# Kernel tuning notes

Measured on AMD Instinct MI355X. Metric: run time of the kernel, lower is better.

The kernel has to match this reference:

```python
import jax, jax.numpy as jnp
import numpy as np

NEG_SLOPE = 0.2  # PyG GATConv default leaky_relu slope
EPS = 1e-16


def setup_inputs() -> dict:
    key = jax.random.key(0)
    ks = jax.random.split(key, 8)
    N, E, F = 50000, 1600000, 128
    L, H, C = 3, 4, 32  # layers, heads, per-head channels; H*C == F
    Dh = 32             # MLP hidden (== hidden_channels)
    x = jax.random.normal(ks[0], (N, F), jnp.float32)
    edge_index = jax.random.randint(ks[1], (2, E), 0, N, jnp.int32)
    W = jax.random.normal(ks[2], (L, F, H * C), jnp.float32) * 0.1
    att_src = jax.random.normal(ks[3], (L, H, C), jnp.float32) * 0.1
    att_dst = jax.random.normal(ks[4], (L, H, C), jnp.float32) * 0.1
    b_conv = jnp.zeros((L, H * C), jnp.float32)
    W1 = jax.random.normal(ks[5], (F + H * C, Dh), jnp.float32) * 0.1
    b1 = jnp.zeros((Dh,), jnp.float32)
    W2 = jax.random.normal(ks[6], (Dh, 1), jnp.float32) * 0.1
    b2 = jnp.zeros((1,), jnp.float32)
    return {"x": x, "edge_index": edge_index, "W": W, "att_src": att_src,
            "att_dst": att_dst, "b_conv": b_conv, "W1": W1, "b1": b1,
            "W2": W2, "b2": b2}


def _gat_layer(x, src, dst, W, a_s, a_d, b, N):
    H, C = a_s.shape
    h = (x @ W).reshape(N, H, C)                      # [N,H,C]
    alpha_s = jnp.sum(h * a_s, axis=-1)               # [N,H]
    alpha_d = jnp.sum(h * a_d, axis=-1)               # [N,H]
    e = jax.nn.leaky_relu(alpha_s[src] + alpha_d[dst], NEG_SLOPE)  # [E,H]
    # segment softmax over incoming edges of each dst node
    m = jax.ops.segment_max(e, dst, num_segments=N)
    ex = jnp.exp(e - m[dst])
    s = jax.ops.segment_sum(ex, dst, num_segments=N)
    a = ex / (s[dst] + EPS)                           # [E,H]
    out = jax.ops.segment_sum(h[src] * a[:, :, None], dst, num_segments=N)
    return out.reshape(N, H * C) + b


def reference(x, edge_index, W, att_src, att_dst, b_conv, W1, b1, W2, b2):
    N = x.shape[0]
    loops = jnp.arange(N, dtype=edge_index.dtype)
    src = jnp.concatenate([edge_index[0], loops])  # PyG GATConv adds self loops
    dst = jnp.concatenate([edge_index[1], loops])
    x0 = x
    for l in range(W.shape[0]):
        x = _gat_layer(x, src, dst, W[l], att_src[l], att_dst[l], b_conv[l], N)
    h = jnp.concatenate([x, x0], axis=-1)
    h = jax.nn.relu(h @ W1 + b1)
    return jax.nn.sigmoid(h @ W2 + b2)
```

## Files before the change

### kernel.cpp

```cpp
#include <hip/hip_runtime.h>

#define NEG_SLOPE 0.2f
#define EPSF 1e-16f

typedef unsigned int uint;
typedef unsigned short ushort;
typedef __attribute__((ext_vector_type(8))) short short8;
typedef __attribute__((ext_vector_type(4))) float floatx4;

static __device__ __forceinline__ ushort f2bf(float f) {
    uint u = __float_as_uint(f);
    return (ushort)((u + 0x7FFFu + ((u >> 16) & 1u)) >> 16);
}
static __device__ __forceinline__ uint pack2(float a, float b) {
    return (uint)f2bf(a) | ((uint)f2bf(b) << 16);
}
static __device__ __forceinline__ float bf_lo(uint p) { return __uint_as_float(p << 16); }
static __device__ __forceinline__ float bf_hi(uint p) { return __uint_as_float(p & 0xFFFF0000u); }
static __device__ __forceinline__ short8 u2s8(uint4 v) {
    union { uint4 u; short8 s; } c; c.u = v; return c.s;
}

__global__ __launch_bounds__(256) void prepack_w_kernel(
    const float* __restrict__ W, const float* __restrict__ W1,
    uint4* __restrict__ Wp, uint4* __restrict__ W1p, int L)
{
    int id = blockIdx.x * 256 + threadIdx.x;
    int nW = L * 2048;
    if (id < nW) {
        int l = id >> 11, s = id & 2047;
        int chunk = s >> 7, col = s & 127;
        const float* wp = W + (size_t)l * 16384 + (chunk * 8) * 128 + col;
        uint4 pk;
        pk.x = pack2(wp[0],   wp[128]);
        pk.y = pack2(wp[256], wp[384]);
        pk.z = pack2(wp[512], wp[640]);
        pk.w = pack2(wp[768], wp[896]);
        Wp[id] = pk;
    } else if (id < nW + 1024) {
        int s = id - nW;
        int chunk = s >> 5, col = s & 31;
        const float* wp = W1 + (chunk * 8) * 32 + col;
        uint4 pk;
        pk.x = pack2(wp[0],   wp[32]);
        pk.y = pack2(wp[64],  wp[96]);
        pk.z = pack2(wp[128], wp[160]);
        pk.w = pack2(wp[192], wp[224]);
        W1p[s] = pk;
    }
}

__global__ __launch_bounds__(256) void prepack_x_kernel(
    const float* __restrict__ x, uint4* __restrict__ xb, int N)
{
    int id = blockIdx.x * 256 + threadIdx.x;
    if (id >= N * 16) return;
    int row = id >> 4, c8 = id & 15;
    const float4* xp = (const float4*)(x + (size_t)row * 128 + c8 * 8);
    float4 v0 = xp[0], v1 = xp[1];
    uint4 pk;
    pk.x = pack2(v0.x, v0.y); pk.y = pack2(v0.z, v0.w);
    pk.z = pack2(v1.x, v1.y); pk.w = pack2(v1.z, v1.w);
    xb[id] = pk;
}

#define GA_LDS_BYTES ((2048 + 1040) * 16)
__global__ __launch_bounds__(256) void gemm_alpha_kernel(
    const uint4* __restrict__ xb, const uint4* __restrict__ Wp,
    const float* __restrict__ att_s, const float* __restrict__ att_d,
    uint* __restrict__ h2, float* __restrict__ alpha_s,
    float* __restrict__ alpha_d, int N)
{
    __shared__ __align__(16) char smraw[GA_LDS_BYTES];
    uint4* sW = (uint4*)smraw;
    uint4* sX = sW + 2048;
    float* sD = (float*)smraw;

    const int t = threadIdx.x;
    const int rowBase = blockIdx.x * 64;

#pragma unroll
    for (int i = 0; i < 8; ++i) {
        int slot = t + i * 256;
        sW[slot] = Wp[slot];
    }
#pragma unroll
    for (int i = 0; i < 4; ++i) {
        int f = t + i * 256;
        int row = f >> 4, c8 = f & 15;
        uint4 v = make_uint4(0u, 0u, 0u, 0u);
        if (rowBase + row < N) v = xb[(size_t)(rowBase + row) * 16 + c8];
        sX[c8 * 65 + row] = v;
    }
    __syncthreads();

    const int w = t >> 6, lane = t & 63, q = lane >> 4, l15 = lane & 15;
    short8 a[4];
#pragma unroll
    for (int s = 0; s < 4; ++s)
        a[s] = u2s8(sX[(4 * s + q) * 65 + 16 * w + l15]);

    floatx4 acc[8];
#pragma unroll
    for (int ct = 0; ct < 8; ++ct) acc[ct] = (floatx4){0.f, 0.f, 0.f, 0.f};
#pragma unroll
    for (int ct = 0; ct < 8; ++ct) {
#pragma unroll
        for (int s = 0; s < 4; ++s) {
            short8 b = u2s8(sW[(4 * s + q) * 128 + 16 * ct + l15]);
            acc[ct] = __builtin_amdgcn_mfma_f32_16x16x32_bf16(a[s], b, acc[ct], 0, 0, 0);
        }
    }
    __syncthreads();

#pragma unroll
    for (int ct = 0; ct < 8; ++ct) {
#pragma unroll
        for (int r = 0; r < 4; ++r)
            sD[(16 * w + 4 * q + r) * 129 + 16 * ct + l15] = acc[ct][r];
    }
    __syncthreads();

#pragma unroll
    for (int i = 0; i < 4; ++i) {
        int slot = t + i * 256;
        int row = slot >> 4, c8 = slot & 15;
        if (rowBase + row < N) {
            const float* dp = &sD[row * 129 + c8 * 8];
            uint4 o;
            o.x = pack2(dp[0], dp[1]); o.y = pack2(dp[2], dp[3]);
            o.z = pack2(dp[4], dp[5]); o.w = pack2(dp[6], dp[7]);
            ((uint4*)h2)[(size_t)(rowBase + row) * 16 + c8] = o;
        }
    }
    {
        int row = t & 63, head = t >> 6;
        if (rowBase + row < N) {
            const float* dp = &sD[row * 129 + head * 32];
            const float* asp = att_s + head * 32;
            const float* adp = att_d + head * 32;
            float ps = 0.f, pd = 0.f;
#pragma unroll
            for (int c = 0; c < 32; ++c) { float v = dp[c]; ps += v * asp[c]; pd += v * adp[c]; }
            alpha_s[(size_t)(rowBase + row) * 4 + head] = ps;
            alpha_d[(size_t)(rowBase + row) * 4 + head] = pd;
        }
    }
}

__global__ __launch_bounds__(256) void zero256_kernel(int* __restrict__ p)
{
    p[threadIdx.x] = 0;
}

__global__ __launch_bounds__(256) void bucket_count_kernel(
    const int* __restrict__ ei, int E, int NB, int* __restrict__ bucket_count)
{
    __shared__ int cnt[256];
    cnt[threadIdx.x] = 0;
    __syncthreads();
    const int base = blockIdx.x * 2048 + threadIdx.x;
#pragma unroll
    for (int j = 0; j < 8; ++j) {
        int idx = base + j * 256;
        if (idx < E) atomicAdd(&cnt[ei[E + idx] >> 8], 1);
    }
    __syncthreads();
    int c = cnt[threadIdx.x];
    if (threadIdx.x < NB && c) atomicAdd(&bucket_count[threadIdx.x], c);
}

__global__ __launch_bounds__(256) void bucket_scan_kernel(
    const int* __restrict__ bucket_count, int NB,
    int* __restrict__ bucket_base, int* __restrict__ bucket_cursor,
    int* __restrict__ row_start, int N)
{
    __shared__ int s[256];
    const int t = threadIdx.x;
    int v = (t < NB) ? bucket_count[t] : 0;
    s[t] = v;
    __syncthreads();
    for (int off = 1; off < 256; off <<= 1) {
        int x = s[t];
        int a = (t >= off) ? s[t - off] : 0;
        __syncthreads();
        s[t] = x + a;
        __syncthreads();
    }
    int ex = s[t] - v;
    if (t < NB) { bucket_base[t] = ex; bucket_cursor[t] = ex; }
    if (t == 255) { bucket_base[NB] = s[255]; row_start[N] = s[255]; }
}

__global__ __launch_bounds__(256) void distribute_kernel(
    const int* __restrict__ ei, int E, int NB,
    int* __restrict__ bucket_cursor, uint* __restrict__ bdata)
{
    __shared__ int cnt[256];
    __shared__ int bbase[256];
    cnt[threadIdx.x] = 0;
    __syncthreads();
    const int base = blockIdx.x * 2048 + threadIdx.x;
    int srcs[8], dsts[8], rank[8];
#pragma unroll
    for (int j = 0; j < 8; ++j) {
        int idx = base + j * 256;
        if (idx < E) {
            srcs[j] = ei[idx];
            dsts[j] = ei[E + idx];
            rank[j] = atomicAdd(&cnt[dsts[j] >> 8], 1);
        } else dsts[j] = -1;
    }
    __syncthreads();
    {
        int c = cnt[threadIdx.x];
        bbase[threadIdx.x] = (threadIdx.x < NB && c) ? atomicAdd(&bucket_cursor[threadIdx.x], c) : 0;
    }
    __syncthreads();
#pragma unroll
    for (int j = 0; j < 8; ++j) {
        if (dsts[j] >= 0) {
            int b = dsts[j] >> 8;
            bdata[bbase[b] + rank[j]] = (uint)srcs[j] | ((uint)(dsts[j] & 255) << 16);
        }
    }
}

#define BCAP 12800
__global__ __launch_bounds__(256) void bucket_csr_kernel(
    const uint* __restrict__ bdata, const int* __restrict__ bucket_base,
    int* __restrict__ row_start, ushort* __restrict__ csr_src, int N)
{
    __shared__ int hist[256];
    __shared__ int scn[256];
    __shared__ int cur[256];
    __shared__ ushort buf[BCAP];
    const int b = blockIdx.x;
    const int t = threadIdx.x;
    const int beg = bucket_base[b];
    const int sz = bucket_base[b + 1] - beg;
    hist[t] = 0;
    __syncthreads();
    for (int i = t; i < sz; i += 256) atomicAdd(&hist[bdata[beg + i] >> 16], 1);
    __syncthreads();
    int v = hist[t];
    scn[t] = v;
    __syncthreads();
    for (int off = 1; off < 256; off <<= 1) {
        int x = scn[t];
        int a = (t >= off) ? scn[t - off] : 0;
        __syncthreads();
        scn[t] = x + a;
        __syncthreads();
    }
    int ex = scn[t] - v;
    cur[t] = ex;
    int node = b * 256 + t;
    if (node < N) row_start[node] = beg + ex;
    __syncthreads();
    if (sz <= BCAP) {
        for (int i = t; i < sz; i += 256) {
            uint d = bdata[beg + i];
            int pos = atomicAdd(&cur[d >> 16], 1);
            buf[pos] = (ushort)(d & 0xFFFFu);
        }
        __syncthreads();
        for (int i = t; i < sz; i += 256) csr_src[beg + i] = buf[i];
    } else {
        for (int i = t; i < sz; i += 256) {
            uint d = bdata[beg + i];
            int pos = atomicAdd(&cur[d >> 16], 1);
            csr_src[beg + pos] = (ushort)(d & 0xFFFFu);
        }
    }
}

__global__ __launch_bounds__(256) void agg_csr_kernel(
    const ushort* __restrict__ csr_src, const int* __restrict__ row_start,
    const float* __restrict__ alpha_s, const float* __restrict__ alpha_d,
    const uint* __restrict__ h2, const float* __restrict__ b,
    uint4* __restrict__ outb, int N)
{
    const int g = (blockIdx.x * 256 + threadIdx.x) >> 4;
    const int l = threadIdx.x & 15;
    if (g >= N) return;
    const int head = l >> 2;
    const uint4* h4 = (const uint4*)h2;

    const float ad = alpha_d[g * 4 + head];

    float e = alpha_s[g * 4 + head] + ad;
    e = e > 0.f ? e : NEG_SLOPE * e;
    float ex = __expf(e);
    uint4 q = h4[(size_t)g * 16 + l];
    float a0 = ex * bf_lo(q.x), a1 = ex * bf_hi(q.x);
    float a2 = ex * bf_lo(q.y), a3 = ex * bf_hi(q.y);
    float a4 = ex * bf_lo(q.z), a5 = ex * bf_hi(q.z);
    float a6 = ex * bf_lo(q.w), a7 = ex * bf_hi(q.w);
    float sx = ex;

    const int beg = row_start[g];
    const int end = row_start[g + 1];
    int k = beg;
    for (; k + 2 <= end; k += 2) {
        int s0 = csr_src[k], s1 = csr_src[k + 1];
        float e0 = alpha_s[s0 * 4 + head] + ad;
        float e1 = alpha_s[s1 * 4 + head] + ad;
        uint4 q0 = h4[(size_t)s0 * 16 + l];
        uint4 q1 = h4[(size_t)s1 * 16 + l];
        e0 = e0 > 0.f ? e0 : NEG_SLOPE * e0;
        e1 = e1 > 0.f ? e1 : NEG_SLOPE * e1;
        float x0 = __expf(e0), x1 = __expf(e1);
        a0 += x0 * bf_lo(q0.x) + x1 * bf_lo(q1.x);
        a1 += x0 * bf_hi(q0.x) + x1 * bf_hi(q1.x);
        a2 += x0 * bf_lo(q0.y) + x1 * bf_lo(q1.y);
        a3 += x0 * bf_hi(q0.y) + x1 * bf_hi(q1.y);
        a4 += x0 * bf_lo(q0.z) + x1 * bf_lo(q1.z);
        a5 += x0 * bf_hi(q0.z) + x1 * bf_hi(q1.z);
        a6 += x0 * bf_lo(q0.w) + x1 * bf_lo(q1.w);
        a7 += x0 * bf_hi(q0.w) + x1 * bf_hi(q1.w);
        sx += x0 + x1;
    }
    if (k < end) {
        int s0 = csr_src[k];
        float e0 = alpha_s[s0 * 4 + head] + ad;
        uint4 q0 = h4[(size_t)s0 * 16 + l];
        e0 = e0 > 0.f ? e0 : NEG_SLOPE * e0;
        float x0 = __expf(e0);
        a0 += x0 * bf_lo(q0.x); a1 += x0 * bf_hi(q0.x);
        a2 += x0 * bf_lo(q0.y); a3 += x0 * bf_hi(q0.y);
        a4 += x0 * bf_lo(q0.z); a5 += x0 * bf_hi(q0.z);
        a6 += x0 * bf_lo(q0.w); a7 += x0 * bf_hi(q0.w);
        sx += x0;
    }
    const float inv = 1.f / (sx + EPSF);
    const float4 b0 = ((const float4*)b)[l * 2];
    const float4 b1 = ((const float4*)b)[l * 2 + 1];
    uint4 o;
    o.x = pack2(b0.x + a0 * inv, b0.y + a1 * inv);
    o.y = pack2(b0.z + a2 * inv, b0.w + a3 * inv);
    o.z = pack2(b1.x + a4 * inv, b1.y + a5 * inv);
    o.w = pack2(b1.z + a6 * inv, b1.w + a7 * inv);
    outb[(size_t)g * 16 + l] = o;
}

__global__ __launch_bounds__(256) void mlp_kernel(
    const uint4* __restrict__ xb3, const uint4* __restrict__ xb0,
    const uint4* __restrict__ W1p, const float* __restrict__ b1,
    const float* __restrict__ W2, const float* __restrict__ b2,
    float* __restrict__ out, int N)
{
    __shared__ __align__(16) uint4 sA[32 * 65];
    __shared__ __align__(16) uint4 sB[32 * 32];
    const int t = threadIdx.x;
    const int rowBase = blockIdx.x * 64;

#pragma unroll
    for (int i = 0; i < 8; ++i) {
        int f = t + i * 256;
        int c = f & 31, row = f >> 5;
        uint4 v = make_uint4(0u, 0u, 0u, 0u);
        int grow = rowBase + row;
        if (grow < N)
            v = (c < 16) ? xb3[(size_t)grow * 16 + c]
                         : xb0[(size_t)grow * 16 + (c - 16)];
        sA[c * 65 + row] = v;
    }
#pragma unroll
    for (int i = 0; i < 4; ++i) {
        int slot = t + i * 256;
        sB[slot] = W1p[slot];
    }
    __syncthreads();

    const int w = t >> 6, lane = t & 63, q = lane >> 4, l15 = lane & 15;
    floatx4 acc0 = (floatx4){0.f, 0.f, 0.f, 0.f};
    floatx4 acc1 = (floatx4){0.f, 0.f, 0.f, 0.f};
#pragma unroll
    for (int s = 0; s < 8; ++s) {
        short8 a = u2s8(sA[(4 * s + q) * 65 + 16 * w + l15]);
        acc0 = __builtin_amdgcn_mfma_f32_16x16x32_bf16(a, u2s8(sB[(4 * s + q) * 32 + l15]), acc0, 0, 0, 0);
        acc1 = __builtin_amdgcn_mfma_f32_16x16x32_bf16(a, u2s8(sB[(4 * s + q) * 32 + 16 + l15]), acc1, 0, 0, 0);
    }
    const float b1a = b1[l15], b1b = b1[16 + l15];
    const float w2a = W2[l15], w2b = W2[16 + l15];
    const float b2v = b2[0];
#pragma unroll
    for (int r = 0; r < 4; ++r) {
        int row = rowBase + 16 * w + 4 * q + r;
        float v0 = acc0[r] + b1a; v0 = v0 > 0.f ? v0 : 0.f;
        float v1 = acc1[r] + b1b; v1 = v1 > 0.f ? v1 : 0.f;
        float p = v0 * w2a + v1 * w2b;
        p += __shfl_xor(p, 1);
        p += __shfl_xor(p, 2);
        p += __shfl_xor(p, 4);
        p += __shfl_xor(p, 8);
        if (l15 == 0 && row < N)
            out[row] = 1.f / (1.f + __expf(-(p + b2v)));
    }
}

extern "C" void kernel_launch(void* const* d_in, const int* in_sizes, int n_in,
                              void* d_out, int out_size, void* d_ws, size_t ws_size,
                              hipStream_t stream)
{
    const float* x       = (const float*)d_in[0];
    const int*   ei      = (const int*)d_in[1];
    const float* W       = (const float*)d_in[2];
    const float* att_src = (const float*)d_in[3];
    const float* att_dst = (const float*)d_in[4];
    const float* b_conv  = (const float*)d_in[5];
    const float* W1      = (const float*)d_in[6];
    const float* b1      = (const float*)d_in[7];
    const float* W2      = (const float*)d_in[8];
    const float* b2      = (const float*)d_in[9];
    float* outp = (float*)d_out;

    const int N = in_sizes[0] / 128;
    const int E = in_sizes[1] / 2;
    const int L = in_sizes[2] / (128 * 128);
    const int NB = (N + 255) >> 8;

    char* ws = (char*)d_ws;
    uint*  h2      = (uint*)ws;
    uint4* xb0     = (uint4*)(h2 + (size_t)N * 64);
    uint4* xb      = xb0 + (size_t)N * 16;
    float* alpha_s = (float*)(xb + (size_t)N * 16);
    float* alpha_d = alpha_s + (size_t)N * 4;
    uint4* Wp      = (uint4*)(alpha_d + (size_t)N * 4);
    uint4* W1p     = Wp + (size_t)L * 2048;
    int* bucket_count  = (int*)(W1p + 1024);
    int* bucket_base   = bucket_count + 256;
    int* bucket_cursor = bucket_base + 260;
    int* row_start     = bucket_cursor + 256;
    uint* bdata        = (uint*)(row_start + N + 1);
    ushort* csr_src    = (ushort*)(bdata + E);

    const int nbE = (E + 2047) / 2048;

    prepack_w_kernel<<<(L * 2048 + 1024 + 255) / 256, 256, 0, stream>>>(
        W, W1, Wp, W1p, L);
    prepack_x_kernel<<<(N * 16 + 255) / 256, 256, 0, stream>>>(x, xb0, N);

    zero256_kernel<<<1, 256, 0, stream>>>(bucket_count);
    bucket_count_kernel<<<nbE, 256, 0, stream>>>(ei, E, NB, bucket_count);
    bucket_scan_kernel<<<1, 256, 0, stream>>>(bucket_count, NB, bucket_base,
                                              bucket_cursor, row_start, N);
    distribute_kernel<<<nbE, 256, 0, stream>>>(ei, E, NB, bucket_cursor, bdata);
    bucket_csr_kernel<<<NB, 256, 0, stream>>>(bdata, bucket_base, row_start,
                                              csr_src, N);

    for (int l = 0; l < L; ++l) {
        const uint4* xin = (l == 0) ? xb0 : xb;
        const uint4* Wl  = Wp + (size_t)l * 2048;
        const float* asl = att_src + (size_t)l * 128;
        const float* adl = att_dst + (size_t)l * 128;
        const float* bl  = b_conv + (size_t)l * 128;

        gemm_alpha_kernel<<<(N + 63) / 64, 256, 0, stream>>>(
            xin, Wl, asl, adl, h2, alpha_s, alpha_d, N);

        agg_csr_kernel<<<(N * 16 + 255) / 256, 256, 0, stream>>>(
            csr_src, row_start, alpha_s, alpha_d, h2, bl, xb, N);
    }

    mlp_kernel<<<(N + 63) / 64, 256, 0, stream>>>(
        xb, xb0, W1p, b1, W2, b2, outp, N);
}
```

Measured before the change: 391.6 us.

## Merge prep kernels, use direct global-to-LDS loads, unroll aggregation by four

After: 387.7 us. Within noise of the previous version (-1.0%).

```diff
diff --git a/kernel.cpp b/kernel.cpp
--- a/kernel.cpp
+++ b/kernel.cpp
@@ -20,13 +20,21 @@
 static __device__ __forceinline__ short8 u2s8(uint4 v) {
     union { uint4 u; short8 s; } c; c.u = v; return c.s;
 }
-
-__global__ __launch_bounds__(256) void prepack_w_kernel(
+static __device__ __forceinline__ void load_lds16(const void* g, void* l) {
+    __builtin_amdgcn_global_load_lds(
+        (const __attribute__((address_space(1))) void*)g,
+        (__attribute__((address_space(3))) void*)l, 16, 0, 0);
+}
+
+__global__ __launch_bounds__(256) void prep_kernel(
     const float* __restrict__ W, const float* __restrict__ W1,
-    uint4* __restrict__ Wp, uint4* __restrict__ W1p, int L)
+    const float* __restrict__ x, uint4* __restrict__ Wp,
+    uint4* __restrict__ W1p, uint4* __restrict__ xb,
+    int* __restrict__ bucket_count, int L, int N)
 {
     int id = blockIdx.x * 256 + threadIdx.x;
-    int nW = L * 2048;
+    const int nW = L * 2048;
+    const int nX = N * 16;
     if (id < nW) {
         int l = id >> 11, s = id & 2047;
         int chunk = s >> 7, col = s & 127;
@@ -47,21 +55,18 @@
         pk.z = pack2(wp[128], wp[160]);
         pk.w = pack2(wp[192], wp[224]);
         W1p[s] = pk;
-    }
-}
-
-__global__ __launch_bounds__(256) void prepack_x_kernel(
-    const float* __restrict__ x, uint4* __restrict__ xb, int N)
-{
-    int id = blockIdx.x * 256 + threadIdx.x;
-    if (id >= N * 16) return;
-    int row = id >> 4, c8 = id & 15;
-    const float4* xp = (const float4*)(x + (size_t)row * 128 + c8 * 8);
-    float4 v0 = xp[0], v1 = xp[1];
-    uint4 pk;
-    pk.x = pack2(v0.x, v0.y); pk.y = pack2(v0.z, v0.w);
-    pk.z = pack2(v1.x, v1.y); pk.w = pack2(v1.z, v1.w);
-    xb[id] = pk;
+    } else if (id < nW + 1024 + nX) {
+        int xid = id - nW - 1024;
+        int row = xid >> 4, c8 = xid & 15;
+        const float4* xp = (const float4*)(x + (size_t)row * 128 + c8 * 8);
+        float4 v0 = xp[0], v1 = xp[1];
+        uint4 pk;
+        pk.x = pack2(v0.x, v0.y); pk.y = pack2(v0.z, v0.w);
+        pk.z = pack2(v1.x, v1.y); pk.w = pack2(v1.z, v1.w);
+        xb[xid] = pk;
+    } else if (id < nW + 1024 + nX + 256) {
+        bucket_count[id - nW - 1024 - nX] = 0;
+    }
 }
 
 #define GA_LDS_BYTES ((2048 + 1040) * 16)
@@ -77,13 +82,13 @@
     float* sD = (float*)smraw;
 
     const int t = threadIdx.x;
+    const int wb = t & ~63;
     const int rowBase = blockIdx.x * 64;
 
 #pragma unroll
-    for (int i = 0; i < 8; ++i) {
-        int slot = t + i * 256;
-        sW[slot] = Wp[slot];
-    }
+    for (int i = 0; i < 8; ++i)
+        load_lds16(Wp + i * 256 + t, sW + i * 256 + wb);
+
 #pragma unroll
     for (int i = 0; i < 4; ++i) {
         int f = t + i * 256;
@@ -148,11 +153,6 @@
     }
 }
 
-__global__ __launch_bounds__(256) void zero256_kernel(int* __restrict__ p)
-{
-    p[threadIdx.x] = 0;
-}
-
 __global__ __launch_bounds__(256) void bucket_count_kernel(
     const int* __restrict__ ei, int E, int NB, int* __restrict__ bucket_count)
 {
@@ -302,26 +302,34 @@
     const int beg = row_start[g];
     const int end = row_start[g + 1];
     int k = beg;
-    for (; k + 2 <= end; k += 2) {
+    for (; k + 4 <= end; k += 4) {
         int s0 = csr_src[k], s1 = csr_src[k + 1];
+        int s2 = csr_src[k + 2], s3 = csr_src[k + 3];
+        uint4 q0 = h4[(size_t)s0 * 16 + l];
+        uint4 q1 = h4[(size_t)s1 * 16 + l];
+        uint4 q2 = h4[(size_t)s2 * 16 + l];
+        uint4 q3 = h4[(size_t)s3 * 16 + l];
         float e0 = alpha_s[s0 * 4 + head] + ad;
         float e1 = alpha_s[s1 * 4 + head] + ad;
-        uint4 q0 = h4[(size_t)s0 * 16 + l];
-        uint4 q1 = h4[(size_t)s1 * 16 + l];
+        float e2 = alpha_s[s2 * 4 + head] + ad;
+        float e3 = alpha_s[s3 * 4 + head] + ad;
         e0 = e0 > 0.f ? e0 : NEG_SLOPE * e0;
         e1 = e1 > 0.f ? e1 : NEG_SLOPE * e1;
+        e2 = e2 > 0.f ? e2 : NEG_SLOPE * e2;
+        e3 = e3 > 0.f ? e3 : NEG_SLOPE * e3;
         float x0 = __expf(e0), x1 = __expf(e1);
-        a0 += x0 * bf_lo(q0.x) + x1 * bf_lo(q1.x);
-        a1 += x0 * bf_hi(q0.x) + x1 * bf_hi(q1.x);
-        a2 += x0 * bf_lo(q0.y) + x1 * bf_lo(q1.y);
-        a3 += x0 * bf_hi(q0.y) + x1 * bf_hi(q1.y);
-        a4 += x0 * bf_lo(q0.z) + x1 * bf_lo(q1.z);
-        a5 += x0 * bf_hi(q0.z) + x1 * bf_hi(q1.z);
-        a6 += x0 * bf_lo(q0.w) + x1 * bf_lo(q1.w);
-        a7 += x0 * bf_hi(q0.w) + x1 * bf_hi(q1.w);
-        sx += x0 + x1;
-    }
-    if (k < end) {
+        float x2 = __expf(e2), x3 = __expf(e3);
+        a0 += x0 * bf_lo(q0.x) + x1 * bf_lo(q1.x) + x2 * bf_lo(q2.x) + x3 * bf_lo(q3.x);
+        a1 += x0 * bf_hi(q0.x) + x1 * bf_hi(q1.x) + x2 * bf_hi(q2.x) + x3 * bf_hi(q3.x);
+        a2 += x0 * bf_lo(q0.y) + x1 * bf_lo(q1.y) + x2 * bf_lo(q2.y) + x3 * bf_lo(q3.y);
+        a3 += x0 * bf_hi(q0.y) + x1 * bf_hi(q1.y) + x2 * bf_hi(q2.y) + x3 * bf_hi(q3.y);
+        a4 += x0 * bf_lo(q0.z) + x1 * bf_lo(q1.z) + x2 * bf_lo(q2.z) + x3 * bf_lo(q3.z);
+        a5 += x0 * bf_hi(q0.z) + x1 * bf_hi(q1.z) + x2 * bf_hi(q2.z) + x3 * bf_hi(q3.z);
+        a6 += x0 * bf_lo(q0.w) + x1 * bf_lo(q1.w) + x2 * bf_lo(q2.w) + x3 * bf_lo(q3.w);
+        a7 += x0 * bf_hi(q0.w) + x1 * bf_hi(q1.w) + x2 * bf_hi(q2.w) + x3 * bf_hi(q3.w);
+        sx += x0 + x1 + x2 + x3;
+    }
+    for (; k < end; ++k) {
         int s0 = csr_src[k];
         float e0 = alpha_s[s0 * 4 + head] + ad;
         uint4 q0 = h4[(size_t)s0 * 16 + l];
@@ -353,8 +361,12 @@
     __shared__ __align__(16) uint4 sA[32 * 65];
     __shared__ __align__(16) uint4 sB[32 * 32];
     const int t = threadIdx.x;
+    const int wb = t & ~63;
     const int rowBase = blockIdx.x * 64;
 
+#pragma unroll
+    for (int i = 0; i < 4; ++i)
+        load_lds16(W1p + i * 256 + t, sB + i * 256 + wb);
 #pragma unroll
     for (int i = 0; i < 8; ++i) {
         int f = t + i * 256;
@@ -365,11 +377,6 @@
             v = (c < 16) ? xb3[(size_t)grow * 16 + c]
                          : xb0[(size_t)grow * 16 + (c - 16)];
         sA[c * 65 + row] = v;
-    }
-#pragma unroll
-    for (int i = 0; i < 4; ++i) {
-        int slot = t + i * 256;
-        sB[slot] = W1p[slot];
     }
     __syncthreads();
 
@@ -437,12 +444,11 @@
     ushort* csr_src    = (ushort*)(bdata + E);
 
     const int nbE = (E + 2047) / 2048;
-
-    prepack_w_kernel<<<(L * 2048 + 1024 + 255) / 256, 256, 0, stream>>>(
-        W, W1, Wp, W1p, L);
-    prepack_x_kernel<<<(N * 16 + 255) / 256, 256, 0, stream>>>(x, xb0, N);
-
-    zero256_kernel<<<1, 256, 0, stream>>>(bucket_count);
+    const int prepItems = L * 2048 + 1024 + N * 16 + 256;
+
+    prep_kernel<<<(prepItems + 255) / 256, 256, 0, stream>>>(
+        W, W1, x, Wp, W1p, xb0, bucket_count, L, N);
+
     bucket_count_kernel<<<nbE, 256, 0, stream>>>(ei, E, NB, bucket_count);
     bucket_scan_kernel<<<1, 256, 0, stream>>>(bucket_count, NB, bucket_base,
                                               bucket_cursor, row_start, N);
```
